# Kernel tuning notes

Hardware: AMD Instinct MI355X
Metric: run time of the kernel (lower is better)

## Reference

```python
import jax, jax.numpy as jnp
import numpy as np

B, IN, H = 16384, 1024, 1024


def setup_inputs() -> dict:
    key = jax.random.key(0)
    ks = jax.random.split(key, 16)
    stdv = 1.0 / np.sqrt(H)
    u = lambda k, shape: jax.random.uniform(k, shape, jnp.float32, -stdv, stdv)
    return {
        "input": jax.random.normal(ks[0], (B, IN), jnp.float32),
        "prev_h": jax.random.normal(ks[1], (B, H), jnp.float32),
        "prev_c": jax.random.normal(ks[2], (B, H), jnp.float32),
        "weight_xi": u(ks[3], (IN, H)), "weight_hi": u(ks[4], (H, H)),
        "weight_xf": u(ks[5], (IN, H)), "weight_hf": u(ks[6], (H, H)),
        "weight_xu": u(ks[7], (IN, H)), "weight_hu": u(ks[8], (H, H)),
        "weight_xo": u(ks[9], (IN, H)), "weight_ho": u(ks[10], (H, H)),
        "bias_i": u(ks[11], (H,)), "bias_f": u(ks[12], (H,)),
        "bias_o": u(ks[13], (H,)), "bias_u": u(ks[14], (H,)),
    }


def reference(input, prev_h, prev_c,
              weight_xi, weight_hi, weight_xf, weight_hf,
              weight_xu, weight_hu, weight_xo, weight_ho,
              bias_i, bias_f, bias_o, bias_u):
    i = jax.nn.sigmoid(input @ weight_xi + prev_h @ weight_hi + bias_i)
    f = jax.nn.sigmoid(input @ weight_xf + prev_h @ weight_hf + bias_f)
    o = jax.nn.sigmoid(input @ weight_xo + prev_h @ weight_ho + bias_o)
    u = jnp.tanh(input @ weight_xu + prev_h @ weight_hu + bias_u)
    c = f * prev_c + i * u
    h = o * jnp.tanh(c)
    return (h, c)
```

## Files before the change

### kernel.cpp

```cpp
#include <hip/hip_runtime.h>
#include <hip/hip_bf16.h>
#include <stdint.h>
#include <type_traits>


typedef short bf16x8 __attribute__((ext_vector_type(8)));
typedef unsigned short u16x8 __attribute__((ext_vector_type(8)));
typedef float f32x16 __attribute__((ext_vector_type(16)));

__device__ __forceinline__ unsigned short f2bf(float f) {
    union { float f; uint32_t u; } v; v.f = f;
    uint32_t r = v.u + 0x7FFFu + ((v.u >> 16) & 1u);
    return (unsigned short)(r >> 16);
}

__device__ __forceinline__ float fsig(float x) { return 1.0f / (1.0f + __expf(-x)); }
__device__ __forceinline__ float ftanh(float x) { return 2.0f * fsig(2.0f * x) - 1.0f; }

__global__ __launch_bounds__(256) void pack_a_kernel(const float* __restrict__ input,
                                                     const float* __restrict__ prev_h,
                                                     unsigned short* __restrict__ Apk) {
    long idx = (long)blockIdx.x * 256 + threadIdx.x;
    long e0 = idx * 8;
    int b = (int)(e0 >> 11);
    int k = (int)(e0 & 2047);
    const float* src = (k < 1024) ? (input + (size_t)b * 1024 + k)
                                  : (prev_h + (size_t)b * 1024 + (k - 1024));
    float4 lo = *(const float4*)src;
    float4 hi = *(const float4*)(src + 4);
    u16x8 o;
    o[0] = f2bf(lo.x); o[1] = f2bf(lo.y); o[2] = f2bf(lo.z); o[3] = f2bf(lo.w);
    o[4] = f2bf(hi.x); o[5] = f2bf(hi.y); o[6] = f2bf(hi.z); o[7] = f2bf(hi.w);
    *(u16x8*)(Apk + e0) = o;
}

__global__ __launch_bounds__(256) void pack_b_kernel(
        const float* __restrict__ wxi, const float* __restrict__ wxf,
        const float* __restrict__ wxo, const float* __restrict__ wxu,
        const float* __restrict__ whi, const float* __restrict__ whf,
        const float* __restrict__ who, const float* __restrict__ whu,
        unsigned short* __restrict__ Bpk) {
    int idx = blockIdx.x * 256 + threadIdx.x;
    int g  = idx >> 18;
    int r  = idx & 262143;
    int kc = r >> 10;
    int j  = r & 1023;
    const float* wx = (g == 0) ? wxi : (g == 1) ? wxf : (g == 2) ? wxo : wxu;
    const float* wh = (g == 0) ? whi : (g == 1) ? whf : (g == 2) ? who : whu;
    int k0 = kc * 8;
    const float* src = (k0 < 1024) ? (wx + (size_t)k0 * 1024 + j)
                                   : (wh + (size_t)(k0 - 1024) * 1024 + j);
    u16x8 o;
#pragma unroll
    for (int t = 0; t < 8; ++t) o[t] = f2bf(src[(size_t)t * 1024]);
    *(u16x8*)(Bpk + (((size_t)(g * 1024 + j)) << 11) + k0) = o;
}


#define GLL(gp, lp) __builtin_amdgcn_global_load_lds( \
        (__attribute__((address_space(1))) void*)(gp), \
        (__attribute__((address_space(3))) void*)(lp), 16, 0, 0)

#define BAR() do { asm volatile("" ::: "memory"); __builtin_amdgcn_s_barrier(); \
                   asm volatile("" ::: "memory"); } while (0)

__global__ __launch_bounds__(512, 2) void lstm_gemm_kernel(
        const unsigned short* __restrict__ Apk,
        const unsigned short* __restrict__ Bpk,
        const float* __restrict__ prev_c,
        const float* __restrict__ bi, const float* __restrict__ bf_,
        const float* __restrict__ bo, const float* __restrict__ bu,
        float* __restrict__ out_h, float* __restrict__ out_c) {
    __shared__ __align__(16) unsigned char smem[131072];
    const int tid = threadIdx.x;
    const int w = tid >> 6, l = tid & 63;
    const int l31 = l & 31, l5 = l >> 5;
    const int wr = w >> 1, wc = w & 1;

    const int bid = blockIdx.x;
    const int sw = ((bid & 7) << 7) + (bid >> 3);
    const int tileRow = sw & 63, tileCol = sw >> 6;
    const int rowBase = tileRow * 256;
    const int jBase = tileCol * 64;

    int aoff[2][2], boff[4][2];
#pragma unroll
    for (int m = 0; m < 2; ++m)
#pragma unroll
        for (int ks = 0; ks < 2; ++ks)
            aoff[m][ks] = (wr * 2 + m) * 2048 + (ks * 2 + l5) * 512 + l31 * 16;
#pragma unroll
    for (int g = 0; g < 4; ++g)
#pragma unroll
        for (int ks = 0; ks < 2; ++ks)
            boff[g][ks] = 16384 + g * 4096 + wc * 2048 + (ks * 2 + l5) * 512 + l31 * 16;

    const unsigned short* aSq0 = Apk + (size_t)(rowBase + w * 32 + l31) * 2048 + (0 * 2 + l5) * 8;
    const unsigned short* aSq1 = Apk + (size_t)(rowBase + w * 32 + l31) * 2048 + (1 * 2 + l5) * 8;
    const size_t bRow = (size_t)((w >> 1) * 1024 + jBase + (w & 1) * 32 + l31) << 11;
    const unsigned short* bSq0 = Bpk + bRow + (0 * 2 + l5) * 8;
    const unsigned short* bSq1 = Bpk + bRow + (1 * 2 + l5) * 8;
    const int aD0 = w * 2048, aD1 = w * 2048 + 1024;
    const int bD0 = 16384 + (w >> 1) * 4096 + (w & 1) * 2048;
    const int bD1 = bD0 + 1024;

#define STAGE4(T) do { const int _bb = ((T) & 3) * 32768; \
        GLL(aSq0 + (size_t)(T) * 32, smem + _bb + aD0); \
        GLL(aSq1 + (size_t)(T) * 32, smem + _bb + aD1); \
        GLL(bSq0 + (size_t)(T) * 32, smem + _bb + bD0); \
        GLL(bSq1 + (size_t)(T) * 32, smem + _bb + bD1); } while (0)

    f32x16 acc[2][4];
#pragma unroll
    for (int m = 0; m < 2; ++m)
#pragma unroll
        for (int g = 0; g < 4; ++g)
#pragma unroll
            for (int q = 0; q < 16; ++q) acc[m][g][q] = 0.f;

    STAGE4(0); STAGE4(1);
    asm volatile("s_waitcnt vmcnt(4)" ::: "memory");
    BAR();

    auto slice = [&](int t, auto vnc, auto stgc) {
        constexpr int VN = decltype(vnc)::value;
        constexpr bool STG = decltype(stgc)::value;
        const int bt = (t & 3) * 32768;
        if constexpr (STG) STAGE4(t + 2);
        bf16x8 av[2][2], bv[4][2];
#pragma unroll
        for (int m = 0; m < 2; ++m)
#pragma unroll
            for (int ks = 0; ks < 2; ++ks)
                av[m][ks] = *(const bf16x8*)(smem + bt + aoff[m][ks]);
#pragma unroll
        for (int g = 0; g < 4; ++g)
#pragma unroll
            for (int ks = 0; ks < 2; ++ks)
                bv[g][ks] = *(const bf16x8*)(smem + bt + boff[g][ks]);
#pragma unroll
        for (int ks = 0; ks < 2; ++ks)
#pragma unroll
            for (int m = 0; m < 2; ++m)
#pragma unroll
                for (int g = 0; g < 4; ++g)
                    acc[m][g] = __builtin_amdgcn_mfma_f32_32x32x16_bf16(
                        av[m][ks], bv[g][ks], acc[m][g], 0, 0, 0);
        if constexpr (VN == 4)      asm volatile("s_waitcnt vmcnt(4)" ::: "memory");
        else if constexpr (VN == 0) asm volatile("s_waitcnt vmcnt(0)" ::: "memory");
        if constexpr (VN >= 0) BAR();
    };

    using c4 = std::integral_constant<int, 4>;
    using c0 = std::integral_constant<int, 0>;
    using cm = std::integral_constant<int, -1>;
    using bT = std::integral_constant<bool, true>;
    using bF = std::integral_constant<bool, false>;

#pragma unroll 1
    for (int t = 0; t < 62; ++t) slice(t, c4{}, bT{});
    slice(62, c0{}, bF{});
    slice(63, cm{}, bF{});

    const int colIdx = jBase + wc * 32 + l31;
    const float vbi = bi[colIdx], vbf = bf_[colIdx], vbo = bo[colIdx], vbu = bu[colIdx];
    const int rowB = rowBase + wr * 64 + 4 * l5;
#pragma unroll
    for (int m = 0; m < 2; ++m) {
#pragma unroll
        for (int q = 0; q < 16; ++q) {
            const int row = rowB + m * 32 + (q & 3) + 8 * (q >> 2);
            const size_t idx = (size_t)row * 1024 + colIdx;
            float zi = acc[m][0][q] + vbi;
            float zf = acc[m][1][q] + vbf;
            float zo = acc[m][2][q] + vbo;
            float zu = acc[m][3][q] + vbu;
            float iv = fsig(zi), fv = fsig(zf), ov = fsig(zo), uv = ftanh(zu);
            float cv = fv * prev_c[idx] + iv * uv;
            out_c[idx] = cv;
            out_h[idx] = ov * ftanh(cv);
        }
    }
#undef STAGE4
}

extern "C" void kernel_launch(void* const* d_in, const int* in_sizes, int n_in,
                              void* d_out, int out_size, void* d_ws, size_t ws_size,
                              hipStream_t stream) {
    const float* input  = (const float*)d_in[0];
    const float* prev_h = (const float*)d_in[1];
    const float* prev_c = (const float*)d_in[2];
    const float* wxi = (const float*)d_in[3];
    const float* whi = (const float*)d_in[4];
    const float* wxf = (const float*)d_in[5];
    const float* whf = (const float*)d_in[6];
    const float* wxu = (const float*)d_in[7];
    const float* whu = (const float*)d_in[8];
    const float* wxo = (const float*)d_in[9];
    const float* who = (const float*)d_in[10];
    const float* bi  = (const float*)d_in[11];
    const float* bf_ = (const float*)d_in[12];
    const float* bo  = (const float*)d_in[13];
    const float* bu  = (const float*)d_in[14];

    unsigned short* Apk = (unsigned short*)d_ws;
    unsigned short* Bpk = (unsigned short*)((char*)d_ws + (size_t)67108864);

    float* out_h = (float*)d_out;
    float* out_c = out_h + (size_t)16384 * 1024;

    pack_a_kernel<<<dim3(16384), dim3(256), 0, stream>>>(input, prev_h, Apk);
    pack_b_kernel<<<dim3(4096), dim3(256), 0, stream>>>(wxi, wxf, wxo, wxu,
                                                        whi, whf, who, whu, Bpk);
    lstm_gemm_kernel<<<dim3(1024), dim3(512), 0, stream>>>(Apk, Bpk, prev_c,
                                                           bi, bf_, bo, bu, out_h, out_c);
}
```

Measured before the change: 403.8 us.

## Pre-tile packed A and B so each GEMM k-step loads contiguous blocks

The pack kernels now write A and B in a tile-major order that matches exactly what each GEMM block stages into LDS per k-step. Each wave's global_load_lds then reads contiguous 1KB chunks instead of 16-byte pieces strided by a full 4KB row. This is meant to improve DRAM/L2 locality and coalescing in the main GEMM. The cost is more scattered reads in the pack kernels, and correctness depends on the new index mapping matching the LDS layout exactly.

```diff
diff --git a/kernel.cpp b/kernel.cpp
--- a/kernel.cpp
+++ b/kernel.cpp
@@ -19,19 +19,19 @@
 
 __global__ __launch_bounds__(256) void pack_a_kernel(const float* __restrict__ input,
                                                      const float* __restrict__ prev_h,
-                                                     unsigned short* __restrict__ Apk) {
-    long idx = (long)blockIdx.x * 256 + threadIdx.x;
-    long e0 = idx * 8;
-    int b = (int)(e0 >> 11);
-    int k = (int)(e0 & 2047);
-    const float* src = (k < 1024) ? (input + (size_t)b * 1024 + k)
-                                  : (prev_h + (size_t)b * 1024 + (k - 1024));
+                                                     unsigned short* __restrict__ Apk2) {
+    int u = blockIdx.x * 256 + threadIdx.x;
+    int l = u & 63, q = (u >> 6) & 1, rg = (u >> 7) & 7, t = (u >> 10) & 63, rt = u >> 16;
+    int row = rt * 256 + rg * 32 + (l & 31);
+    int k0 = t * 32 + (q * 2 + (l >> 5)) * 8;
+    const float* src = (k0 < 1024) ? (input + (size_t)row * 1024 + k0)
+                                   : (prev_h + (size_t)row * 1024 + (k0 - 1024));
     float4 lo = *(const float4*)src;
     float4 hi = *(const float4*)(src + 4);
     u16x8 o;
     o[0] = f2bf(lo.x); o[1] = f2bf(lo.y); o[2] = f2bf(lo.z); o[3] = f2bf(lo.w);
     o[4] = f2bf(hi.x); o[5] = f2bf(hi.y); o[6] = f2bf(hi.z); o[7] = f2bf(hi.w);
-    *(u16x8*)(Apk + e0) = o;
+    *(u16x8*)(Apk2 + (size_t)u * 8) = o;
 }
 
 __global__ __launch_bounds__(256) void pack_b_kernel(
@@ -39,21 +39,20 @@
         const float* __restrict__ wxo, const float* __restrict__ wxu,
         const float* __restrict__ whi, const float* __restrict__ whf,
         const float* __restrict__ who, const float* __restrict__ whu,
-        unsigned short* __restrict__ Bpk) {
-    int idx = blockIdx.x * 256 + threadIdx.x;
-    int g  = idx >> 18;
-    int r  = idx & 262143;
-    int kc = r >> 10;
-    int j  = r & 1023;
+        unsigned short* __restrict__ Bpk2) {
+    int u = blockIdx.x * 256 + threadIdx.x;
+    int l = u & 63, q = (u >> 6) & 1, ch = (u >> 7) & 1, g = (u >> 8) & 3,
+        t = (u >> 10) & 63, ct = u >> 16;
     const float* wx = (g == 0) ? wxi : (g == 1) ? wxf : (g == 2) ? wxo : wxu;
     const float* wh = (g == 0) ? whi : (g == 1) ? whf : (g == 2) ? who : whu;
-    int k0 = kc * 8;
+    int j = ct * 64 + ch * 32 + (l & 31);
+    int k0 = t * 32 + (q * 2 + (l >> 5)) * 8;
     const float* src = (k0 < 1024) ? (wx + (size_t)k0 * 1024 + j)
                                    : (wh + (size_t)(k0 - 1024) * 1024 + j);
     u16x8 o;
 #pragma unroll
-    for (int t = 0; t < 8; ++t) o[t] = f2bf(src[(size_t)t * 1024]);
-    *(u16x8*)(Bpk + (((size_t)(g * 1024 + j)) << 11) + k0) = o;
+    for (int e = 0; e < 8; ++e) o[e] = f2bf(src[(size_t)e * 1024]);
+    *(u16x8*)(Bpk2 + (size_t)u * 8) = o;
 }
 
 
@@ -65,8 +64,8 @@
                    asm volatile("" ::: "memory"); } while (0)
 
 __global__ __launch_bounds__(512, 2) void lstm_gemm_kernel(
-        const unsigned short* __restrict__ Apk,
-        const unsigned short* __restrict__ Bpk,
+        const unsigned short* __restrict__ Apk2,
+        const unsigned short* __restrict__ Bpk2,
         const float* __restrict__ prev_c,
         const float* __restrict__ bi, const float* __restrict__ bf_,
         const float* __restrict__ bo, const float* __restrict__ bu,
@@ -95,20 +94,18 @@
         for (int ks = 0; ks < 2; ++ks)
             boff[g][ks] = 16384 + g * 4096 + wc * 2048 + (ks * 2 + l5) * 512 + l31 * 16;
 
-    const unsigned short* aSq0 = Apk + (size_t)(rowBase + w * 32 + l31) * 2048 + (0 * 2 + l5) * 8;
-    const unsigned short* aSq1 = Apk + (size_t)(rowBase + w * 32 + l31) * 2048 + (1 * 2 + l5) * 8;
-    const size_t bRow = (size_t)((w >> 1) * 1024 + jBase + (w & 1) * 32 + l31) << 11;
-    const unsigned short* bSq0 = Bpk + bRow + (0 * 2 + l5) * 8;
-    const unsigned short* bSq1 = Bpk + bRow + (1 * 2 + l5) * 8;
-    const int aD0 = w * 2048, aD1 = w * 2048 + 1024;
-    const int bD0 = 16384 + (w >> 1) * 4096 + (w & 1) * 2048;
-    const int bD1 = bD0 + 1024;
+    const unsigned short* aSrc = Apk2 + (size_t)tileRow * 64 * 8192 + w * 1024 + l * 8;
+    const unsigned short* bSrc = Bpk2 + (size_t)tileCol * 64 * 8192
+                               + (w >> 1) * 2048 + (w & 1) * 1024 + l * 8;
+    const int aD = w * 2048;
+    const int bD = 16384 + (w >> 1) * 4096 + (w & 1) * 2048;
 
 #define STAGE4(T) do { const int _bb = ((T) & 3) * 32768; \
-        GLL(aSq0 + (size_t)(T) * 32, smem + _bb + aD0); \
-        GLL(aSq1 + (size_t)(T) * 32, smem + _bb + aD1); \
-        GLL(bSq0 + (size_t)(T) * 32, smem + _bb + bD0); \
-        GLL(bSq1 + (size_t)(T) * 32, smem + _bb + bD1); } while (0)
+        const size_t _o = (size_t)(T) * 8192; \
+        GLL(aSrc + _o,       smem + _bb + aD); \
+        GLL(aSrc + _o + 512, smem + _bb + aD + 1024); \
+        GLL(bSrc + _o,       smem + _bb + bD); \
+        GLL(bSrc + _o + 512, smem + _bb + bD + 1024); } while (0)
 
     f32x16 acc[2][4];
 #pragma unroll
@@ -203,15 +200,15 @@
     const float* bo  = (const float*)d_in[13];
     const float* bu  = (const float*)d_in[14];
 
-    unsigned short* Apk = (unsigned short*)d_ws;
-    unsigned short* Bpk = (unsigned short*)((char*)d_ws + (size_t)67108864);
+    unsigned short* Apk2 = (unsigned short*)d_ws;
+    unsigned short* Bpk2 = (unsigned short*)((char*)d_ws + (size_t)67108864);
 
     float* out_h = (float*)d_out;
     float* out_c = out_h + (size_t)16384 * 1024;
 
-    pack_a_kernel<<<dim3(16384), dim3(256), 0, stream>>>(input, prev_h, Apk);
+    pack_a_kernel<<<dim3(16384), dim3(256), 0, stream>>>(input, prev_h, Apk2);
     pack_b_kernel<<<dim3(4096), dim3(256), 0, stream>>>(wxi, wxf, wxo, wxu,
-                                                        whi, whf, who, whu, Bpk);
-    lstm_gemm_kernel<<<dim3(1024), dim3(512), 0, stream>>>(Apk, Bpk, prev_c,
+                                                        whi, whf, who, whu, Bpk2);
+    lstm_gemm_kernel<<<dim3(1024), dim3(512), 0, stream>>>(Apk2, Bpk2, prev_c,
                                                            bi, bf_, bo, bu, out_h, out_c);
 }
```

New measurement: 349.9 us. 1.15x faster.
